# Performance work log

Hardware: AMD Instinct MI355X
Metric: run time of the kernel (lower is better)

Reference implementation:

```python
import jax, jax.numpy as jnp
import numpy as np

D_C = 16  # c // 4 with c = 64
BN_EPS = 1e-5


def _block(x, w, b, g, beta, m, v, a):
    """Conv2Dblock with 1x1 conv: pointwise conv -> BatchNorm2d (inference) -> PReLU."""
    y = jnp.einsum('oi,bift->boft', w, x) + b[None, :, None, None]
    scale = (g / jnp.sqrt(v + BN_EPS))[None, :, None, None]
    y = (y - m[None, :, None, None]) * scale + beta[None, :, None, None]
    return jnp.where(y >= 0, y, a * y)  # PReLU, single shared slope


def _asa(inp, fqkv, tqk, proj):
    b, c, f, t = inp.shape
    scale = 1.0 / np.sqrt(D_C)
    neg = -jnp.finfo(inp.dtype).max

    # frequency attention
    f_qkv = _block(inp, *fqkv)                      # [b, 3*d_c interleaved, f, t]
    f_qkv = f_qkv.reshape(b, D_C, 3, f, t)          # '(c k)' split, k fastest
    qf, kf, v = f_qkv[:, :, 0], f_qkv[:, :, 1], f_qkv[:, :, 2]
    f_score = jnp.einsum('bcft,bcyt->btfy', qf, kf) * scale
    f_score = jax.nn.softmax(f_score, axis=-1)
    f_out = jnp.einsum('btfy,bcyt->bcft', f_score, v)

    # causal time attention
    t_qk = _block(inp, *tqk)                        # [b, 2*d_c interleaved, f, t]
    t_qk = t_qk.reshape(b, D_C, 2, f, t)
    qt, kt = t_qk[:, :, 0], t_qk[:, :, 1]
    t_score = jnp.einsum('bcft,bcfy->bfty', qt, kt) * scale
    causal_mask = jnp.triu(jnp.ones((t, t), dtype=bool), 1)  # strictly upper => future
    t_score = jnp.where(causal_mask[None, None], neg, t_score)
    t_score = jax.nn.softmax(t_score, axis=-1)
    t_out = jnp.einsum('bfty,bcfy->bcft', t_score, f_out)

    out = _block(t_out, *proj)
    return out + inp


def setup_inputs() -> dict:
    key = jax.random.key(0)
    ks = jax.random.split(key, 24)
    B, C, F, T = 2, 64, 257, 500
    dc = D_C

    def conv_params(ki, kb, out_ch, in_ch):
        w = jax.random.normal(ki, (out_ch, in_ch), jnp.float32) * (1.0 / np.sqrt(in_ch))
        b = jax.random.normal(kb, (out_ch,), jnp.float32) * 0.02
        return w, b

    inp = jax.random.normal(ks[0], (B, C, F, T), jnp.float32)

    fqkv_w, fqkv_b = conv_params(ks[1], ks[2], 3 * dc, C)
    fqkv_g = 1.0 + 0.1 * jax.random.uniform(ks[3], (3 * dc,), jnp.float32)
    fqkv_beta = 0.02 * jax.random.normal(ks[4], (3 * dc,), jnp.float32)
    fqkv_m = 0.02 * jax.random.normal(ks[5], (3 * dc,), jnp.float32)
    fqkv_v = 0.9 + 0.2 * jax.random.uniform(ks[6], (3 * dc,), jnp.float32)
    fqkv_a = jnp.full((1,), 0.25, jnp.float32)

    tqk_w, tqk_b = conv_params(ks[7], ks[8], 2 * dc, C)
    tqk_g = 1.0 + 0.1 * jax.random.uniform(ks[9], (2 * dc,), jnp.float32)
    tqk_beta = 0.02 * jax.random.normal(ks[10], (2 * dc,), jnp.float32)
    tqk_m = 0.02 * jax.random.normal(ks[11], (2 * dc,), jnp.float32)
    tqk_v = 0.9 + 0.2 * jax.random.uniform(ks[12], (2 * dc,), jnp.float32)
    tqk_a = jnp.full((1,), 0.25, jnp.float32)

    proj_w, proj_b = conv_params(ks[13], ks[14], C, dc)
    proj_g = 1.0 + 0.1 * jax.random.uniform(ks[15], (C,), jnp.float32)
    proj_beta = 0.02 * jax.random.normal(ks[16], (C,), jnp.float32)
    proj_m = 0.02 * jax.random.normal(ks[17], (C,), jnp.float32)
    proj_v = 0.9 + 0.2 * jax.random.uniform(ks[18], (C,), jnp.float32)
    proj_a = jnp.full((1,), 0.25, jnp.float32)

    return dict(inp=inp,
                fqkv_w=fqkv_w, fqkv_b=fqkv_b, fqkv_g=fqkv_g, fqkv_beta=fqkv_beta,
                fqkv_m=fqkv_m, fqkv_v=fqkv_v, fqkv_a=fqkv_a,
                tqk_w=tqk_w, tqk_b=tqk_b, tqk_g=tqk_g, tqk_beta=tqk_beta,
                tqk_m=tqk_m, tqk_v=tqk_v, tqk_a=tqk_a,
                proj_w=proj_w, proj_b=proj_b, proj_g=proj_g, proj_beta=proj_beta,
                proj_m=proj_m, proj_v=proj_v, proj_a=proj_a)


def reference(inp, fqkv_w, fqkv_b, fqkv_g, fqkv_beta, fqkv_m, fqkv_v, fqkv_a,
              tqk_w, tqk_b, tqk_g, tqk_beta, tqk_m, tqk_v, tqk_a,
              proj_w, proj_b, proj_g, proj_beta, proj_m, proj_v, proj_a):
    return _asa(inp,
                (fqkv_w, fqkv_b, fqkv_g, fqkv_beta, fqkv_m, fqkv_v, fqkv_a),
                (tqk_w, tqk_b, tqk_g, tqk_beta, tqk_m, tqk_v, tqk_a),
                (proj_w, proj_b, proj_g, proj_beta, proj_m, proj_v, proj_a))
```

## Files before the change

### kernel.cpp

```cpp
#include <hip/hip_runtime.h>

#define BB 2
#define CIN 64
#define FD 257
#define TD 500
#define FT (FD*TD)
#define EPS 1e-5f
#define NEGINF (-3.0e38f)
#define FDP 260
#define FQT_PLANE (TD*FDP)
#define FOT_PLANE (TD*FDP)
#define LOG2E 1.44269504088896f
#define EXP2F(x) __builtin_amdgcn_exp2f(x)

typedef _Float16 half_t;
typedef half_t half2_t __attribute__((ext_vector_type(2)));
typedef half_t half4 __attribute__((ext_vector_type(4)));
typedef float  f32x4 __attribute__((ext_vector_type(4)));

__global__ __launch_bounds__(256) void stage1_kernel(
    const float* __restrict__ x,
    const float* __restrict__ fw, const float* __restrict__ fb_,
    const float* __restrict__ fg, const float* __restrict__ fbe,
    const float* __restrict__ fm, const float* __restrict__ fv_,
    const float* __restrict__ fa,
    const float* __restrict__ tw, const float* __restrict__ tb_,
    const float* __restrict__ tg, const float* __restrict__ tbe,
    const float* __restrict__ tm, const float* __restrict__ tv_,
    const float* __restrict__ ta,
    half_t* __restrict__ fq, half_t* __restrict__ tq)
{
    __shared__ half_t Wh[80][68];
    __shared__ float  Bl[80];
    __shared__ half_t Ob[4][32][80];
    const int tid = threadIdx.x;
    for (int idx = tid; idx < 80*64; idx += 256) {
        const int o = idx >> 6, i = idx & 63;
        float sc, wv;
        if (o < 48) { sc = fg[o]*rsqrtf(fv_[o]+EPS); wv = fw[o*64+i]; }
        else { const int o2 = o-48; sc = tg[o2]*rsqrtf(tv_[o2]+EPS); wv = tw[o2*64+i]; }
        Wh[o][i] = (half_t)(wv*sc);
    }
    if (tid < 80) {
        const int o = tid;
        if (o < 48) Bl[o] = (fb_[o]-fm[o])*(fg[o]*rsqrtf(fv_[o]+EPS)) + fbe[o];
        else { const int o2 = o-48; Bl[o] = (tb_[o2]-tm[o2])*(tg[o2]*rsqrtf(tv_[o2]+EPS)) + tbe[o2]; }
    }
    __syncthreads();
    const float af = fa[0], at = ta[0];
    const int w = tid >> 6, lane = tid & 63;
    const int lmod = lane & 15, ldiv = lane >> 4;
    const int b  = blockIdx.x / 1004;
    const int nb = blockIdx.x % 1004;
    const long n0 = (long)nb*128;

    half4 a[5][4];
    #pragma unroll
    for (int ot = 0; ot < 5; ++ot)
        #pragma unroll
        for (int ks = 0; ks < 4; ++ks)
            a[ot][ks] = *(const half4*)&Wh[16*ot + lmod][16*ks + 4*ldiv];
    f32x4 bias[5];
    #pragma unroll
    for (int ot = 0; ot < 5; ++ot)
        #pragma unroll
        for (int r = 0; r < 4; ++r)
            bias[ot][r] = Bl[16*ot + 4*ldiv + r];

    const float* xplane = x + (long)b*CIN*FT;
    half4 bfr[2][4];
    #pragma unroll
    for (int pt = 0; pt < 2; ++pt) {
        const long p = n0 + 32*w + 16*pt + lmod;
        const long pc = (p < FT) ? p : (FT-1);
        const float* xp = xplane + pc;
        #pragma unroll
        for (int ks = 0; ks < 4; ++ks) {
            #pragma unroll
            for (int e = 0; e < 4; ++e) {
                const int ch = 16*ks + 4*ldiv + e;
                bfr[pt][ks][e] = (half_t)xp[(long)ch*FT];
            }
        }
    }
    #pragma unroll
    for (int pt = 0; pt < 2; ++pt) {
        const int pl = 16*pt + lmod;
        const int msk = ((pl >> 2) & 3) << 2;
        #pragma unroll
        for (int ot = 0; ot < 5; ++ot) {
            f32x4 acc = bias[ot];
            #pragma unroll
            for (int ks = 0; ks < 4; ++ks)
                acc = __builtin_amdgcn_mfma_f32_16x16x16f16(a[ot][ks], bfr[pt][ks], acc, 0, 0, 0);
            const float alpha = (ot < 3) ? af : at;
            half4 hv;
            #pragma unroll
            for (int r = 0; r < 4; ++r) {
                float v = acc[r];
                v = v >= 0.f ? v : alpha*v;
                hv[r] = (half_t)v;
            }
            *(half4*)&Ob[w][pl][(16*ot + 4*ldiv) ^ msk] = hv;
        }
    }
    const int pr = lane & 7, og0 = lane >> 3;
    const long pbase = n0 + 32*w + 4*pr;
    if (pbase < FT) {
        const int msk = (pr & 3) << 2;
        #pragma unroll
        for (int i = 0; i < 10; ++i) {
            const int o = og0 + 8*i;
            half4 hv;
            #pragma unroll
            for (int e = 0; e < 4; ++e) hv[e] = Ob[w][4*pr + e][o ^ msk];
            half_t* dst = (o < 48) ? (fq + ((long)b*48 + o)*FT + pbase)
                                   : (tq + ((long)b*32 + (o-48))*FT + pbase);
            *(half4*)dst = hv;
        }
    }
}

__global__ __launch_bounds__(256) void transpose_h2h_kernel(
    const half_t* __restrict__ src, half_t* __restrict__ dst,
    int R, int C, int CS, int RP)
{
    __shared__ half_t tile[64][68];
    const int plane = blockIdx.x;
    const int rb = blockIdx.y*64, cb = blockIdx.z*64;
    const half_t* s = src + (long)plane*R*CS;
    half_t* d = dst + (long)plane*C*RP;
    const int q4 = (threadIdx.x & 15)*4;
    const int wl = threadIdx.x >> 4;
    #pragma unroll
    for (int p = 0; p < 4; ++p) {
        const int r = rb + wl + 16*p;
        const int c = cb + q4;
        half4 v = {(half_t)0.f,(half_t)0.f,(half_t)0.f,(half_t)0.f};
        if (r < R) {
            const half_t* srow = s + (long)r*CS;
            if (c + 3 < C) v = *(const half4*)(srow + c);
            else {
                #pragma unroll
                for (int e = 0; e < 4; ++e) if (c+e < C) v[e] = srow[c+e];
            }
        }
        *(half4*)&tile[wl + 16*p][q4] = v;
    }
    __syncthreads();
    #pragma unroll
    for (int p = 0; p < 4; ++p) {
        const int c = cb + wl + 16*p;
        if (c >= C) continue;
        const int r0 = rb + q4;
        half4 o;
        #pragma unroll
        for (int e = 0; e < 4; ++e) o[e] = tile[q4 + e][wl + 16*p];
        half_t* drow = d + (long)c*RP;
        if (r0 + 3 < RP) *(half4*)(drow + r0) = o;
        else {
            #pragma unroll
            for (int e = 0; e < 4; ++e) if (r0+e < RP) drow[r0+e] = o[e];
        }
    }
}

__global__ __launch_bounds__(512) void fattn_kernel(
    const half_t* __restrict__ fqT, half_t* __restrict__ foT)
{
    __shared__ half_t KT[272*20];
    __shared__ half_t QT[272*20];
    __shared__ half_t Vs[16*280];
    const int tid = threadIdx.x;
    const int b = blockIdx.x / TD, t = blockIdx.x % TD;
    const half_t* base = fqT + (long)b*48*FQT_PLANE + (long)t*FDP;
    const half_t qsc = (half_t)(0.25f*LOG2E);
    for (int s = tid; s < 48*68; s += 512) {
        const int c3 = s / 68, j = s - c3*68;
        const int f0 = 4*j;
        half4 v = {(half_t)0.f,(half_t)0.f,(half_t)0.f,(half_t)0.f};
        if (f0 < FDP) v = *(const half4*)(base + (long)c3*FQT_PLANE + f0);
        const int c = c3 / 3, wh = c3 - 3*c;
        if (wh == 0) {
            #pragma unroll
            for (int e = 0; e < 4; ++e) QT[(f0+e)*20 + c] = v[e]*qsc;
        } else if (wh == 1) {
            #pragma unroll
            for (int e = 0; e < 4; ++e) KT[(f0+e)*20 + c] = v[e];
        } else {
            *(half4*)&Vs[c*280 + f0] = v;
        }
    }
    __syncthreads();
    const int w = tid >> 6, lane = tid & 63;
    const int lmod = lane & 15, ldiv = lane >> 4;
    for (int ft = w; ft < 17; ft += 8) {
        const int f0 = 16*ft;
        const half4 qb = *(const half4*)&QT[(f0+lmod)*20 + 4*ldiv];
        f32x4 o = {0.f,0.f,0.f,0.f};
        float m = NEGINF, l = 0.f;
        for (int yt = 0; yt < 16; yt += 2) {
            const int y0 = 16*yt;
            const half4 ka0 = *(const half4*)&KT[(y0   +lmod)*20 + 4*ldiv];
            const half4 ka1 = *(const half4*)&KT[(y0+16+lmod)*20 + 4*ldiv];
            f32x4 s0 = __builtin_amdgcn_mfma_f32_16x16x16f16(
                ka0, qb, (f32x4){0.f,0.f,0.f,0.f}, 0, 0, 0);
            f32x4 s1 = __builtin_amdgcn_mfma_f32_16x16x16f16(
                ka1, qb, (f32x4){0.f,0.f,0.f,0.f}, 0, 0, 0);
            float mt = fmaxf(fmaxf(fmaxf(s0[0],s0[1]), fmaxf(s0[2],s0[3])),
                             fmaxf(fmaxf(s1[0],s1[1]), fmaxf(s1[2],s1[3])));
            mt = fmaxf(mt, __shfl_xor(mt, 16, 64));
            mt = fmaxf(mt, __shfl_xor(mt, 32, 64));
            const float mn = fmaxf(m, mt);
            const float alpha = EXP2F(m - mn);
            half4 pb0, pb1; float ps = 0.f;
            #pragma unroll
            for (int r = 0; r < 4; ++r) {
                const float p0 = EXP2F(s0[r] - mn);
                const float p1 = EXP2F(s1[r] - mn);
                pb0[r] = (half_t)p0; pb1[r] = (half_t)p1;
                ps += p0 + p1;
            }
            ps += __shfl_xor(ps, 16, 64);
            ps += __shfl_xor(ps, 32, 64);
            l = l*alpha + ps;  m = mn;
            o[0] *= alpha; o[1] *= alpha; o[2] *= alpha; o[3] *= alpha;
            const half4 va0 = *(const half4*)&Vs[lmod*280 + y0      + 4*ldiv];
            const half4 va1 = *(const half4*)&Vs[lmod*280 + y0 + 16 + 4*ldiv];
            o = __builtin_amdgcn_mfma_f32_16x16x16f16(va0, pb0, o, 0, 0, 0);
            o = __builtin_amdgcn_mfma_f32_16x16x16f16(va1, pb1, o, 0, 0, 0);
        }
        {
            const int y0 = 256;
            const half4 ka = *(const half4*)&KT[(y0+lmod)*20 + 4*ldiv];
            f32x4 s = __builtin_amdgcn_mfma_f32_16x16x16f16(
                ka, qb, (f32x4){0.f,0.f,0.f,0.f}, 0, 0, 0);
            #pragma unroll
            for (int r = 0; r < 4; ++r)
                if (y0 + 4*ldiv + r >= FD) s[r] = NEGINF;
            float mt = fmaxf(fmaxf(s[0],s[1]), fmaxf(s[2],s[3]));
            mt = fmaxf(mt, __shfl_xor(mt, 16, 64));
            mt = fmaxf(mt, __shfl_xor(mt, 32, 64));
            const float mn = fmaxf(m, mt);
            const float alpha = EXP2F(m - mn);
            half4 pb; float ps = 0.f;
            #pragma unroll
            for (int r = 0; r < 4; ++r) {
                const float p = EXP2F(s[r] - mn);
                pb[r] = (half_t)p; ps += p;
            }
            ps += __shfl_xor(ps, 16, 64);
            ps += __shfl_xor(ps, 32, 64);
            l = l*alpha + ps;  m = mn;
            o[0] *= alpha; o[1] *= alpha; o[2] *= alpha; o[3] *= alpha;
            const half4 va = *(const half4*)&Vs[lmod*280 + y0 + 4*ldiv];
            o = __builtin_amdgcn_mfma_f32_16x16x16f16(va, pb, o, 0, 0, 0);
        }
        const float inv = 1.f/l;
        const int f = f0 + lmod;
        if (f < FD) {
            #pragma unroll
            for (int r = 0; r < 4; ++r) {
                const int c = 4*ldiv + r;
                foT[((long)(b*16 + c)*TD + t)*FDP + f] = (half_t)(o[r]*inv);
            }
        }
    }
}

__global__ __launch_bounds__(512) void tattn_kernel(
    const half_t* __restrict__ tq, const half_t* __restrict__ fo,
    float* __restrict__ tout)
{
    extern __shared__ half_t lds[];
    half_t* KT  = lds;
    half_t* QT  = KT + 512*20;
    half_t* FOs = QT + 512*20;
    const int tid = threadIdx.x;
    const int b = blockIdx.x / FD, f = blockIdx.x % FD;
    const half_t* qbase = tq + (long)b*32*FT + (long)f*TD;
    const half_t* fbase = fo + (long)b*16*FT + (long)f*TD;
    const half_t qsc = (half_t)(0.25f*LOG2E);
    for (int idx = tid; idx < 16*128; idx += 512) {
        const int c = idx >> 7, y4 = (idx & 127)*4;
        half4 qv = {(half_t)0.f,(half_t)0.f,(half_t)0.f,(half_t)0.f};
        half4 kv = qv, fv = qv;
        if (y4 + 3 < TD) {
            qv = *(const half4*)(qbase + (long)(2*c  )*FT + y4);
            kv = *(const half4*)(qbase + (long)(2*c+1)*FT + y4);
            fv = *(const half4*)(fbase + (long)c*FT + y4);
        }
        #pragma unroll
        for (int e = 0; e < 4; ++e) {
            QT[(y4+e)*20 + c] = qv[e]*qsc;
            KT[(y4+e)*20 + c] = kv[e];
        }
        *(half4*)&FOs[c*520 + y4] = fv;
    }
    __syncthreads();
    const int w = tid >> 6, lane = tid & 63;
    const int lmod = lane & 15, ldiv = lane >> 4;
    const int tts[4] = {w, 15-w, 16+w, 31-w};
    #pragma unroll
    for (int i = 0; i < 4; ++i) {
        const int tt = tts[i];
        const int t0 = 16*tt;
        const half4 qb = *(const half4*)&QT[(t0+lmod)*20 + 4*ldiv];
        f32x4 o = {0.f,0.f,0.f,0.f};
        float m = NEGINF, l = 0.f;
        int yt = 0;
        for (; yt + 1 < tt; yt += 2) {
            const int y0 = 16*yt;
            const half4 ka0 = *(const half4*)&KT[(y0   +lmod)*20 + 4*ldiv];
            const half4 ka1 = *(const half4*)&KT[(y0+16+lmod)*20 + 4*ldiv];
            f32x4 s0 = __builtin_amdgcn_mfma_f32_16x16x16f16(
                ka0, qb, (f32x4){0.f,0.f,0.f,0.f}, 0, 0, 0);
            f32x4 s1 = __builtin_amdgcn_mfma_f32_16x16x16f16(
                ka1, qb, (f32x4){0.f,0.f,0.f,0.f}, 0, 0, 0);
            float mt = fmaxf(fmaxf(fmaxf(s0[0],s0[1]), fmaxf(s0[2],s0[3])),
                             fmaxf(fmaxf(s1[0],s1[1]), fmaxf(s1[2],s1[3])));
            mt = fmaxf(mt, __shfl_xor(mt, 16, 64));
            mt = fmaxf(mt, __shfl_xor(mt, 32, 64));
            const float mn = fmaxf(m, mt);
            const float alpha = EXP2F(m - mn);
            half4 pb0, pb1; float ps = 0.f;
            #pragma unroll
            for (int r = 0; r < 4; ++r) {
                const float p0 = EXP2F(s0[r] - mn);
                const float p1 = EXP2F(s1[r] - mn);
                pb0[r] = (half_t)p0; pb1[r] = (half_t)p1;
                ps += p0 + p1;
            }
            ps += __shfl_xor(ps, 16, 64);
            ps += __shfl_xor(ps, 32, 64);
            l = l*alpha + ps;  m = mn;
            o[0] *= alpha; o[1] *= alpha; o[2] *= alpha; o[3] *= alpha;
            const half4 fa0 = *(const half4*)&FOs[lmod*520 + y0      + 4*ldiv];
            const half4 fa1 = *(const half4*)&FOs[lmod*520 + y0 + 16 + 4*ldiv];
            o = __builtin_amdgcn_mfma_f32_16x16x16f16(fa0, pb0, o, 0, 0, 0);
            o = __builtin_amdgcn_mfma_f32_16x16x16f16(fa1, pb1, o, 0, 0, 0);
        }
        if (yt < tt) {
            const int y0 = 16*yt;
            const half4 ka0 = *(const half4*)&KT[(y0   +lmod)*20 + 4*ldiv];
            const half4 ka1 = *(const half4*)&KT[(y0+16+lmod)*20 + 4*ldiv];
            f32x4 s0 = __builtin_amdgcn_mfma_f32_16x16x16f16(
                ka0, qb, (f32x4){0.f,0.f,0.f,0.f}, 0, 0, 0);
            f32x4 s1 = __builtin_amdgcn_mfma_f32_16x16x16f16(
                ka1, qb, (f32x4){0.f,0.f,0.f,0.f}, 0, 0, 0);
            #pragma unroll
            for (int r = 0; r < 4; ++r)
                if (4*ldiv + r > lmod) s1[r] = NEGINF;
            float mt = fmaxf(fmaxf(fmaxf(s0[0],s0[1]), fmaxf(s0[2],s0[3])),
                             fmaxf(fmaxf(s1[0],s1[1]), fmaxf(s1[2],s1[3])));
            mt = fmaxf(mt, __shfl_xor(mt, 16, 64));
            mt = fmaxf(mt, __shfl_xor(mt, 32, 64));
            const float mn = fmaxf(m, mt);
            const float alpha = EXP2F(m - mn);
            half4 pb0, pb1; float ps = 0.f;
            #pragma unroll
            for (int r = 0; r < 4; ++r) {
                const float p0 = EXP2F(s0[r] - mn);
                const float p1 = EXP2F(s1[r] - mn);
                pb0[r] = (half_t)p0; pb1[r] = (half_t)p1;
                ps += p0 + p1;
            }
            ps += __shfl_xor(ps, 16, 64);
            ps += __shfl_xor(ps, 32, 64);
            l = l*alpha + ps;  m = mn;
            o[0] *= alpha; o[1] *= alpha; o[2] *= alpha; o[3] *= alpha;
            const half4 fa0 = *(const half4*)&FOs[lmod*520 + y0      + 4*ldiv];
            const half4 fa1 = *(const half4*)&FOs[lmod*520 + y0 + 16 + 4*ldiv];
            o = __builtin_amdgcn_mfma_f32_16x16x16f16(fa0, pb0, o, 0, 0, 0);
            o = __builtin_amdgcn_mfma_f32_16x16x16f16(fa1, pb1, o, 0, 0, 0);
        } else {
            const int y0 = 16*tt;
            const half4 ka = *(const half4*)&KT[(y0+lmod)*20 + 4*ldiv];
            f32x4 s = __builtin_amdgcn_mfma_f32_16x16x16f16(
                ka, qb, (f32x4){0.f,0.f,0.f,0.f}, 0, 0, 0);
            #pragma unroll
            for (int r = 0; r < 4; ++r)
                if (4*ldiv + r > lmod) s[r] = NEGINF;
            float mt = fmaxf(fmaxf(s[0],s[1]), fmaxf(s[2],s[3]));
            mt = fmaxf(mt, __shfl_xor(mt, 16, 64));
            mt = fmaxf(mt, __shfl_xor(mt, 32, 64));
            const float mn = fmaxf(m, mt);
            const float alpha = EXP2F(m - mn);
            half4 pb; float ps = 0.f;
            #pragma unroll
            for (int r = 0; r < 4; ++r) {
                const float p = EXP2F(s[r] - mn);
                pb[r] = (half_t)p; ps += p;
            }
            ps += __shfl_xor(ps, 16, 64);
            ps += __shfl_xor(ps, 32, 64);
            l = l*alpha + ps;  m = mn;
            o[0] *= alpha; o[1] *= alpha; o[2] *= alpha; o[3] *= alpha;
            const half4 fa4 = *(const half4*)&FOs[lmod*520 + y0 + 4*ldiv];
            o = __builtin_amdgcn_mfma_f32_16x16x16f16(fa4, pb, o, 0, 0, 0);
        }
        const float inv = 1.f/l;
        const int t = t0 + lmod;
        if (t < TD) {
            #pragma unroll
            for (int r = 0; r < 4; ++r) {
                const int c = 4*ldiv + r;
                tout[((long)(b*16 + c)*FD + f)*TD + t] = o[r]*inv;
            }
        }
    }
}

__global__ __launch_bounds__(256) void proj_kernel(
    const float* __restrict__ tout, const float* __restrict__ x,
    const float* __restrict__ pw, const float* __restrict__ pb_,
    const float* __restrict__ pg, const float* __restrict__ pbe,
    const float* __restrict__ pm, const float* __restrict__ pv_,
    const float* __restrict__ pa,
    float* __restrict__ out)
{
    __shared__ float PW[32*16];
    __shared__ float PB[32];
    const int tid = threadIdx.x;
    const int cg   = blockIdx.x & 1;
    const int bidx = blockIdx.x >> 1;
    const int ob   = cg*32;
    for (int idx = tid; idx < 32*16; idx += 256) {
        const int ol = idx >> 4;
        const int o = ob + ol;
        PW[idx] = pw[o*16 + (idx & 15)]*(pg[o]*rsqrtf(pv_[o]+EPS));
    }
    if (tid < 32) {
        const int o = ob + tid;
        PB[tid] = (pb_[o]-pm[o])*(pg[o]*rsqrtf(pv_[o]+EPS)) + pbe[o];
    }
    __syncthreads();
    const float ap = pa[0];
    const int og = tid >> 6, lane = tid & 63;
    const int b  = bidx / 502;
    const int nb = bidx % 502;
    const long n0 = (long)nb*256 + lane*4;
    if (n0 >= FT) return;
    float4 acc[8];
    #pragma unroll
    for (int j = 0; j < 8; ++j) {
        const float bv = PB[og*8+j];
        acc[j] = make_float4(bv, bv, bv, bv);
    }
    const float* tb = tout + (long)b*16*FT + n0;
    for (int cc = 0; cc < 16; cc += 4) {
        const float* tc = tb + (long)cc*FT;
        const float4 t0 = *(const float4*)(tc);
        const float4 t1 = *(const float4*)(tc + FT);
        const float4 t2 = *(const float4*)(tc + 2*FT);
        const float4 t3 = *(const float4*)(tc + 3*FT);
        #pragma unroll
        for (int j = 0; j < 8; ++j) {
            const float4 wv = *(const float4*)&PW[(og*8+j)*16 + cc];
            acc[j].x += wv.x*t0.x + wv.y*t1.x + wv.z*t2.x + wv.w*t3.x;
            acc[j].y += wv.x*t0.y + wv.y*t1.y + wv.z*t2.y + wv.w*t3.y;
            acc[j].z += wv.x*t0.z + wv.y*t1.z + wv.z*t2.z + wv.w*t3.z;
            acc[j].w += wv.x*t0.w + wv.y*t1.w + wv.z*t2.w + wv.w*t3.w;
        }
    }
    #pragma unroll
    for (int j = 0; j < 8; ++j) {
        const int o = ob + og*8 + j;
        float4 v = acc[j];
        v.x = v.x >= 0.f ? v.x : ap*v.x;
        v.y = v.y >= 0.f ? v.y : ap*v.y;
        v.z = v.z >= 0.f ? v.z : ap*v.z;
        v.w = v.w >= 0.f ? v.w : ap*v.w;
        const long gi = (long)(b*64 + o)*FT + n0;
        const float4 xv = *(const float4*)(x + gi);
        v.x += xv.x; v.y += xv.y; v.z += xv.z; v.w += xv.w;
        *(float4*)(out + gi) = v;
    }
}

extern "C" void kernel_launch(void* const* d_in, const int* in_sizes, int n_in,
                              void* d_out, int out_size, void* d_ws, size_t ws_size,
                              hipStream_t stream)
{
    const float* x     = (const float*)d_in[0];
    const float* fw    = (const float*)d_in[1];
    const float* fb_   = (const float*)d_in[2];
    const float* fg    = (const float*)d_in[3];
    const float* fbe   = (const float*)d_in[4];
    const float* fm    = (const float*)d_in[5];
    const float* fv_   = (const float*)d_in[6];
    const float* fa    = (const float*)d_in[7];
    const float* tw    = (const float*)d_in[8];
    const float* tb_   = (const float*)d_in[9];
    const float* tg    = (const float*)d_in[10];
    const float* tbe   = (const float*)d_in[11];
    const float* tm    = (const float*)d_in[12];
    const float* tv_   = (const float*)d_in[13];
    const float* ta    = (const float*)d_in[14];
    const float* pw    = (const float*)d_in[15];
    const float* pb_   = (const float*)d_in[16];
    const float* pg    = (const float*)d_in[17];
    const float* pbe   = (const float*)d_in[18];
    const float* pm    = (const float*)d_in[19];
    const float* pv_   = (const float*)d_in[20];
    const float* pa    = (const float*)d_in[21];
    float* out = (float*)d_out;

    char* base = (char*)d_ws;
    const size_t szA = (size_t)BB*48*FT*sizeof(half_t);
    const size_t szB = (size_t)BB*16*FT*sizeof(half_t);
    const size_t szC = (size_t)BB*32*FT*sizeof(half_t);
    const size_t szD = (size_t)96*FQT_PLANE*sizeof(half_t);
    const size_t need = szA + szB + szC + szD;
    if (ws_size < need) return;
    half_t* fqh  = (half_t*)base;
    half_t* foTh = (half_t*)base;
    half_t* foh  = (half_t*)(base + szA);
    half_t* tqh  = (half_t*)(base + szA + szB);
    half_t* fqTh = (half_t*)(base + szA + szB + szC);
    float*  tout = (float*)(base + szA + szB + szC);

    stage1_kernel<<<dim3(BB*1004), dim3(256), 0, stream>>>(
        x, fw, fb_, fg, fbe, fm, fv_, fa, tw, tb_, tg, tbe, tm, tv_, ta, fqh, tqh);

    transpose_h2h_kernel<<<dim3(BB*48, 5, 8), dim3(256), 0, stream>>>(
        fqh, fqTh, FD, TD, TD, FDP);

    fattn_kernel<<<dim3(BB*TD), dim3(512), 0, stream>>>(fqTh, foTh);

    transpose_h2h_kernel<<<dim3(BB*16, 8, 5), dim3(256), 0, stream>>>(
        foTh, foh, TD, FD, FDP, TD);

    const int tlds = (512*20*2 + 16*520)*(int)sizeof(half_t);
    (void)hipFuncSetAttribute(reinterpret_cast<const void*>(tattn_kernel),
                        hipFuncAttributeMaxDynamicSharedMemorySize, tlds);
    tattn_kernel<<<dim3(BB*FD), dim3(512), tlds, stream>>>(tqh, foh, tout);

    proj_kernel<<<dim3(BB*502*2), dim3(256), 0, stream>>>(
        tout, x, pw, pb_, pg, pbe, pm, pv_, pa, out);
}
```

Before: 285.2 us.

## Split causal time attention into two query halves per block, load Q to registers

The time-attention kernel now launches two blocks per (batch, frequency). Each block handles half of the query tiles: the first block covers the lower-triangle tiles and only loads keys and values for the first 256 time steps. Q is read straight from global memory into registers instead of being staged transposed in LDS, which shrinks the LDS footprint. This doubles block count and occupancy, at the cost of redundant K/V loads in the second half and uncoalesced scalar Q reads.

```diff
diff --git a/kernel.cpp b/kernel.cpp
--- a/kernel.cpp
+++ b/kernel.cpp
@@ -9,7 +9,6 @@
 #define NEGINF (-3.0e38f)
 #define FDP 260
 #define FQT_PLANE (TD*FDP)
-#define FOT_PLANE (TD*FDP)
 #define LOG2E 1.44269504088896f
 #define EXP2F(x) __builtin_amdgcn_exp2f(x)
 
@@ -274,38 +273,49 @@
 {
     extern __shared__ half_t lds[];
     half_t* KT  = lds;
-    half_t* QT  = KT + 512*20;
-    half_t* FOs = QT + 512*20;
+    half_t* FOs = KT + 512*20;
     const int tid = threadIdx.x;
     const int b = blockIdx.x / FD, f = blockIdx.x % FD;
+    const int h = blockIdx.y;
     const half_t* qbase = tq + (long)b*32*FT + (long)f*TD;
     const half_t* fbase = fo + (long)b*16*FT + (long)f*TD;
     const half_t qsc = (half_t)(0.25f*LOG2E);
-    for (int idx = tid; idx < 16*128; idx += 512) {
-        const int c = idx >> 7, y4 = (idx & 127)*4;
-        half4 qv = {(half_t)0.f,(half_t)0.f,(half_t)0.f,(half_t)0.f};
-        half4 kv = qv, fv = qv;
+    const int shift = h ? 7 : 6;
+    const int nq = 16 << shift;
+    for (int idx = tid; idx < nq; idx += 512) {
+        const int c = idx >> shift;
+        const int y4 = (idx & ((1 << shift) - 1)) * 4;
+        half4 kv = {(half_t)0.f,(half_t)0.f,(half_t)0.f,(half_t)0.f};
+        half4 fv = kv;
         if (y4 + 3 < TD) {
-            qv = *(const half4*)(qbase + (long)(2*c  )*FT + y4);
             kv = *(const half4*)(qbase + (long)(2*c+1)*FT + y4);
             fv = *(const half4*)(fbase + (long)c*FT + y4);
         }
         #pragma unroll
-        for (int e = 0; e < 4; ++e) {
-            QT[(y4+e)*20 + c] = qv[e]*qsc;
-            KT[(y4+e)*20 + c] = kv[e];
-        }
+        for (int e = 0; e < 4; ++e) KT[(y4+e)*20 + c] = kv[e];
         *(half4*)&FOs[c*520 + y4] = fv;
     }
-    __syncthreads();
     const int w = tid >> 6, lane = tid & 63;
     const int lmod = lane & 15, ldiv = lane >> 4;
-    const int tts[4] = {w, 15-w, 16+w, 31-w};
-    #pragma unroll
-    for (int i = 0; i < 4; ++i) {
+    const int tts[2] = { h ? (16 + w) : w, h ? (31 - w) : (15 - w) };
+    half4 qbr[2];
+    #pragma unroll
+    for (int i = 0; i < 2; ++i) {
+        const int t = 16*tts[i] + lmod;
+        #pragma unroll
+        for (int e = 0; e < 4; ++e) {
+            const int c = 4*ldiv + e;
+            half_t qv = (half_t)0.f;
+            if (t < TD) qv = qbase[(long)(2*c)*FT + t];
+            qbr[i][e] = qv * qsc;
+        }
+    }
+    __syncthreads();
+    #pragma unroll
+    for (int i = 0; i < 2; ++i) {
         const int tt = tts[i];
         const int t0 = 16*tt;
-        const half4 qb = *(const half4*)&QT[(t0+lmod)*20 + 4*ldiv];
+        const half4 qb = qbr[i];
         f32x4 o = {0.f,0.f,0.f,0.f};
         float m = NEGINF, l = 0.f;
         int yt = 0;
@@ -531,10 +541,10 @@
     transpose_h2h_kernel<<<dim3(BB*16, 8, 5), dim3(256), 0, stream>>>(
         foTh, foh, TD, FD, FDP, TD);
 
-    const int tlds = (512*20*2 + 16*520)*(int)sizeof(half_t);
+    const int tlds = (512*20 + 16*520)*(int)sizeof(half_t);
     (void)hipFuncSetAttribute(reinterpret_cast<const void*>(tattn_kernel),
                         hipFuncAttributeMaxDynamicSharedMemorySize, tlds);
-    tattn_kernel<<<dim3(BB*FD), dim3(512), tlds, stream>>>(tqh, foh, tout);
+    tattn_kernel<<<dim3(BB*FD, 2), dim3(512), tlds, stream>>>(tqh, foh, tout);
 
     proj_kernel<<<dim3(BB*502*2), dim3(256), 0, stream>>>(
         tout, x, pw, pb_, pg, pbe, pm, pv_, pa, out);
```

Result: no change. 281.2 us (-1.4%).
